# Kernel tuning notes

Hardware: AMD Instinct MI355X
Metric: run time of the kernel (lower is better)

## Reference

```python
import jax, jax.numpy as jnp
import numpy as np

BETA = 0.25
EPS_NORM = 1e-12

def _l2norm(x):
    # F.normalize(x, dim=-1): x / max(||x||, eps)
    n = jnp.sqrt(jnp.sum(x * x, axis=-1, keepdims=True))
    return x / jnp.maximum(n, EPS_NORM)

def setup_inputs() -> dict:
    key = jax.random.key(0)
    k1, k2 = jax.random.split(key)
    z = jax.random.normal(k1, (32, 4096, 256), dtype=jnp.float32)
    # matches nn.Embedding init uniform_(-1/num_embed, 1/num_embed)
    embed_weight = jax.random.uniform(k2, (1024, 256), dtype=jnp.float32,
                                      minval=-1.0 / 1024, maxval=1.0 / 1024)
    return {"z": z, "embed_weight": embed_weight}

def reference(z, embed_weight):
    num_embed, embed_dim = embed_weight.shape
    z_flat = z.reshape(-1, embed_dim)                      # [N, D]
    n_tok = z_flat.shape[0]

    # cosine distance: normalized z (detached) @ normalized codebook^T -> [N, K]
    zn = jax.lax.stop_gradient(_l2norm(z_flat))
    cn = _l2norm(embed_weight)
    d = zn @ cn.T                                          # [N, K]

    # torch sort(dim=1) then indices[:, -1] == argmax along codebook axis
    encoding_indices = jnp.argmax(d, axis=1)               # [N] int

    z_q = embed_weight[encoding_indices].reshape(z.shape)  # gather codebook rows

    # training losses (commitment + codebook)
    sg = jax.lax.stop_gradient
    loss = BETA * jnp.mean((sg(z_q) - z) ** 2) + jnp.mean((z_q - sg(z)) ** 2)

    # straight-through estimator
    z_q_st = z + sg(z_q - z)

    # perplexity from one-hot usage stats (counts instead of dense one-hot)
    counts = jnp.zeros((num_embed,), jnp.float32).at[encoding_indices].add(1.0)
    avg_probs = counts / jnp.float32(n_tok)
    perplexity = jnp.exp(-jnp.sum(avg_probs * jnp.log(avg_probs + 1e-10)))

    return z_q_st, loss, perplexity, encoding_indices
```

## Files before the change

### kernel.cpp

```cpp
#include <hip/hip_runtime.h>
#include <math.h>

#define N_TOK   131072
#define DIM     256
#define K_CODE  1024
#define MARGIN1 3e-2f
#define MARGIN2 2e-3f

#define WS_COUNTS   0
#define WS_LOSSFIX  4096
#define WS_RCOUNT2  4104
#define WS_RCOUNT1  4108
#define WS_PART     8192
#define WS_FIDX     20480
#define WS_RLIST2   1048576
#define WS_RLIST1   1572864
#define WS_BEXT     2097152

#define CHUNK_BYTES 49152

#define OUT_LOSS  33554432
#define OUT_PERP  33554433
#define OUT_IDX   33554434

typedef __bf16 bf16x8 __attribute__((ext_vector_type(8)));
typedef float  f32x4  __attribute__((ext_vector_type(4)));

static __device__ __forceinline__ unsigned short f2bf(float f) {
    unsigned int u = __float_as_uint(f);
    u += 0x7FFFu + ((u >> 16) & 1u);
    return (unsigned short)(u >> 16);
}
static __device__ __forceinline__ float bf2f(unsigned short h) {
    return __uint_as_float(((unsigned int)h) << 16);
}

static __device__ __forceinline__ void load_lds16(const void* g, void* l) {
    __builtin_amdgcn_global_load_lds(
        (const __attribute__((address_space(1))) unsigned int*)g,
        (__attribute__((address_space(3))) unsigned int*)l, 16, 0, 0);
}

__global__ void vq_pack(const float* __restrict__ embed, unsigned short* __restrict__ bext,
                        int* __restrict__ wshdr) {
    __shared__ float cs[4][DIM];
    const int tid  = threadIdx.x;
    const int w    = tid >> 6;
    const int lane = tid & 63;
    const int k0   = blockIdx.x * 4;

    if (blockIdx.x == 0) {
        for (int i = tid; i < 5120; i += 256) wshdr[i] = 0;
    }

    {
        const int k = k0 + w;
        float4 v = *(const float4*)&embed[k * DIM + lane * 4];
        float s = v.x * v.x + v.y * v.y + v.z * v.z + v.w * v.w;
        #pragma unroll
        for (int off = 32; off; off >>= 1) s += __shfl_xor(s, off);
        float inv = 1.0f / fmaxf(sqrtf(s), 1e-12f);
        float4 nv;
        nv.x = v.x * inv; nv.y = v.y * inv; nv.z = v.z * inv; nv.w = v.w * inv;
        *(float4*)&cs[w][lane * 4] = nv;
    }
    __syncthreads();

    for (int t = tid; t < 384; t += 256) {
        int lc  = t / 96;
        int g   = t - lc * 96;
        int k   = k0 + lc;
        int kk0 = g * 8;
        int src, hi;
        if (kk0 < 256)      { src = kk0;       hi = 1; }
        else if (kk0 < 512) { src = kk0 - 256; hi = 0; }
        else                { src = kk0 - 512; hi = 1; }
        unsigned short r[8] __attribute__((aligned(16)));
        #pragma unroll
        for (int j = 0; j < 8; ++j) {
            float vv = cs[lc][src + j];
            unsigned short h = f2bf(vv);
            r[j] = hi ? h : f2bf(vv - bf2f(h));
        }
        int c = k >> 5, kin = k & 31;
        int nt = kin >> 4, col = kin & 15;
        int ks = kk0 >> 5, quad = (kk0 >> 3) & 3;
        size_t dst = (size_t)c * CHUNK_BYTES + (size_t)(((nt * 24 + ks) * 64) + quad * 16 + col) * 16;
        *(float4*)((char*)bext + dst) = *(const float4*)r;
    }
}

__launch_bounds__(256, 4)
__global__ void vq_argmax1(const float* __restrict__ z,
                           const unsigned short* __restrict__ bext,
                           const float* __restrict__ embed,
                           int* __restrict__ fidx,
                           int* __restrict__ r1count, int* __restrict__ rlist1,
                           float* __restrict__ out, int* __restrict__ counts,
                           double* __restrict__ partials) {
    __shared__ unsigned short bbuf[16384];
    __shared__ double shl[4];

    const int tid  = threadIdx.x;
    const int w    = tid >> 6;
    const int lane = tid & 63;
    const int col  = lane & 15;
    const int quad = lane >> 4;
    const int tokBase = blockIdx.x * 128;

    bf16x8 ah[2][8];
    #pragma unroll
    for (int mt = 0; mt < 2; ++mt) {
        const float* zr = z + (size_t)(tokBase + w * 32 + mt * 16 + col) * DIM;
        #pragma unroll
        for (int ks = 0; ks < 8; ++ks) {
            float4 f0 = *(const float4*)(zr + ks * 32 + quad * 8);
            float4 f1 = *(const float4*)(zr + ks * 32 + quad * 8 + 4);
            float v[8] = {f0.x, f0.y, f0.z, f0.w, f1.x, f1.y, f1.z, f1.w};
            union { bf16x8 v; unsigned short u[8]; } th;
            #pragma unroll
            for (int j = 0; j < 8; ++j) th.u[j] = f2bf(v[j]);
            ah[mt][ks] = th.v;
        }
    }

    float best[2][4], second[2][4];
    int   bidx[2][4];
    #pragma unroll
    for (int mt = 0; mt < 2; ++mt)
        #pragma unroll
        for (int r = 0; r < 4; ++r) { best[mt][r] = -1e30f; second[mt][r] = -1e30f; bidx[mt][r] = 0; }

    for (int cc = 0; cc < 32; cc += 2) {
        __syncthreads();
        {
            #pragma unroll
            for (int i = 0; i < 8; ++i) {
                int lseg = w * 8 + i;
                int sub  = lseg >> 4;
                int l    = lseg & 15;
                int g    = l + ((l & 8) ? 16 : 0);
                load_lds16((const char*)bext + (size_t)(cc + sub) * CHUNK_BYTES
                                             + (size_t)g * 1024 + lane * 16,
                           (char*)bbuf + lseg * 1024);
            }
        }
        __syncthreads();

        #pragma unroll
        for (int sub = 0; sub < 2; ++sub) {
            f32x4 acc[2][2];
            #pragma unroll
            for (int mt = 0; mt < 2; ++mt)
                #pragma unroll
                for (int nt = 0; nt < 2; ++nt) acc[mt][nt] = (f32x4){0.f, 0.f, 0.f, 0.f};

            #pragma unroll
            for (int nt = 0; nt < 2; ++nt) {
                const unsigned short* bb = bbuf + sub * 8192 + nt * 4096;
                #pragma unroll
                for (int ks = 0; ks < 8; ++ks) {
                    bf16x8 b = *(const bf16x8*)&bb[ks * 512 + lane * 8];
                    acc[0][nt] = __builtin_amdgcn_mfma_f32_16x16x32_bf16(ah[0][ks], b, acc[0][nt], 0, 0, 0);
                    acc[1][nt] = __builtin_amdgcn_mfma_f32_16x16x32_bf16(ah[1][ks], b, acc[1][nt], 0, 0, 0);
                }
            }

            #pragma unroll
            for (int nt = 0; nt < 2; ++nt) {
                int code = (cc + sub) * 32 + nt * 16 + col;
                #pragma unroll
                for (int mt = 0; mt < 2; ++mt)
                    #pragma unroll
                    for (int r = 0; r < 4; ++r) {
                        float v = acc[mt][nt][r];
                        if (v > best[mt][r]) { second[mt][r] = best[mt][r]; best[mt][r] = v; bidx[mt][r] = code; }
                        else                 { second[mt][r] = fmaxf(second[mt][r], v); }
                    }
            }
        }
    }

    #pragma unroll
    for (int mt = 0; mt < 2; ++mt)
        #pragma unroll
        for (int r = 0; r < 4; ++r) {
            float B = best[mt][r], S = second[mt][r];
            int   I = bidx[mt][r];
            #pragma unroll
            for (int off = 1; off < 16; off <<= 1) {
                float ob = __shfl_xor(B, off);
                float os = __shfl_xor(S, off);
                int   oi = __shfl_xor(I, off);
                if (ob > B) {
                    S = fmaxf(B, os);
                    B = ob; I = oi;
                } else {
                    if (ob == B && oi < I) I = oi;
                    S = fmaxf(S, ob);
                }
            }
            int flag = (B - S < MARGIN1) ? 1 : 0;
            if (col == 0) {
                int token = tokBase + w * 32 + mt * 16 + quad * 4 + r;
                if (!flag) {
                    fidx[token] = I;
                    out[OUT_IDX + token] = (float)I;
                    atomicAdd(&counts[I], 1);
                } else {
                    int p = atomicAdd(r1count, 1);
                    rlist1[p] = token;
                }
            }
            bidx[mt][r] = I | (flag << 30);
        }

    double lsum = 0.0;
    #pragma unroll
    for (int mt = 0; mt < 2; ++mt)
        #pragma unroll
        for (int r = 0; r < 4; ++r)
            #pragma unroll
            for (int q = 0; q < 4; ++q) {
                int enc = __shfl(bidx[mt][r], q * 16);
                if (enc & (1 << 30)) continue;
                int idxv  = enc;
                int token = tokBase + w * 32 + mt * 16 + q * 4 + r;
                float4 e  = *(const float4*)&embed[(size_t)idxv * DIM + lane * 4];
                float4 zz = *(const float4*)&z[(size_t)token * DIM + lane * 4];
                float4 rr, o;
                rr.x = e.x - zz.x; rr.y = e.y - zz.y; rr.z = e.z - zz.z; rr.w = e.w - zz.w;
                o.x = zz.x + rr.x; o.y = zz.y + rr.y; o.z = zz.z + rr.z; o.w = zz.w + rr.w;
                *(float4*)&out[(size_t)token * DIM + lane * 4] = o;
                lsum += (double)rr.x * rr.x + (double)rr.y * rr.y +
                        (double)rr.z * rr.z + (double)rr.w * rr.w;
            }

    #pragma unroll
    for (int off = 32; off; off >>= 1) lsum += __shfl_down(lsum, off);
    if (lane == 0) shl[w] = lsum;
    __syncthreads();
    if (tid == 0) partials[blockIdx.x] = shl[0] + shl[1] + shl[2] + shl[3];
}

__launch_bounds__(256, 2)
__global__ void vq_redo(const float* __restrict__ z,
                        const unsigned short* __restrict__ bext,
                        const float* __restrict__ embed,
                        const int* __restrict__ r1count, const int* __restrict__ rlist1,
                        int* __restrict__ fidx,
                        int* __restrict__ r2count, int* __restrict__ rlist2,
                        float* __restrict__ out, int* __restrict__ counts,
                        double* __restrict__ partials) {
    __shared__ unsigned short bbuf[CHUNK_BYTES / 2];
    __shared__ double shl[4];

    const int tid  = threadIdx.x;
    const int w    = tid >> 6;
    const int lane = tid & 63;
    const int col  = lane & 15;
    const int quad = lane >> 4;
    const int cnt1 = *r1count;

    double lsum = 0.0;

    for (int base = blockIdx.x * 128; base < cnt1; base += gridDim.x * 128) {
        bf16x8 ah[2][8], al[2][8];
        #pragma unroll
        for (int mt = 0; mt < 2; ++mt) {
            int slot = base + w * 32 + mt * 16 + col;
            int tok  = rlist1[min(slot, cnt1 - 1)];
            const float* zr = z + (size_t)tok * DIM;
            #pragma unroll
            for (int ks = 0; ks < 8; ++ks) {
                float4 f0 = *(const float4*)(zr + ks * 32 + quad * 8);
                float4 f1 = *(const float4*)(zr + ks * 32 + quad * 8 + 4);
                float v[8] = {f0.x, f0.y, f0.z, f0.w, f1.x, f1.y, f1.z, f1.w};
                union { bf16x8 v; unsigned short u[8]; } th, tl;
                #pragma unroll
                for (int j = 0; j < 8; ++j) {
                    unsigned short h = f2bf(v[j]);
                    th.u[j] = h;
                    tl.u[j] = f2bf(v[j] - bf2f(h));
                }
                ah[mt][ks] = th.v;
                al[mt][ks] = tl.v;
            }
        }

        float best[2][4], second[2][4];
        int   bidx[2][4];
        #pragma unroll
        for (int mt = 0; mt < 2; ++mt)
            #pragma unroll
            for (int r = 0; r < 4; ++r) { best[mt][r] = -1e30f; second[mt][r] = -1e30f; bidx[mt][r] = 0; }

        for (int c = 0; c < 32; ++c) {
            __syncthreads();
            {
                const char* gsrc = (const char*)bext + (size_t)c * CHUNK_BYTES;
                #pragma unroll
                for (int i = 0; i < 12; ++i) {
                    int seg = w * 12 + i;
                    load_lds16(gsrc + (size_t)seg * 1024 + lane * 16,
                               (char*)bbuf + seg * 1024);
                }
            }
            __syncthreads();

            f32x4 acc[2][2];
            #pragma unroll
            for (int mt = 0; mt < 2; ++mt)
                #pragma unroll
                for (int nt = 0; nt < 2; ++nt) acc[mt][nt] = (f32x4){0.f, 0.f, 0.f, 0.f};

            #pragma unroll
            for (int nt = 0; nt < 2; ++nt) {
                const unsigned short* bb = bbuf + nt * 24 * 512;
                #pragma unroll
                for (int ks = 0; ks < 8; ++ks) {
                    bf16x8 b = *(const bf16x8*)&bb[ks * 512 + lane * 8];
                    acc[0][nt] = __builtin_amdgcn_mfma_f32_16x16x32_bf16(ah[0][ks], b, acc[0][nt], 0, 0, 0);
                    acc[1][nt] = __builtin_amdgcn_mfma_f32_16x16x32_bf16(ah[1][ks], b, acc[1][nt], 0, 0, 0);
                }
                #pragma unroll
                for (int ks = 0; ks < 8; ++ks) {
                    bf16x8 b = *(const bf16x8*)&bb[(8 + ks) * 512 + lane * 8];
                    acc[0][nt] = __builtin_amdgcn_mfma_f32_16x16x32_bf16(ah[0][ks], b, acc[0][nt], 0, 0, 0);
                    acc[1][nt] = __builtin_amdgcn_mfma_f32_16x16x32_bf16(ah[1][ks], b, acc[1][nt], 0, 0, 0);
                }
                #pragma unroll
                for (int ks = 0; ks < 8; ++ks) {
                    bf16x8 b = *(const bf16x8*)&bb[(16 + ks) * 512 + lane * 8];
                    acc[0][nt] = __builtin_amdgcn_mfma_f32_16x16x32_bf16(al[0][ks], b, acc[0][nt], 0, 0, 0);
                    acc[1][nt] = __builtin_amdgcn_mfma_f32_16x16x32_bf16(al[1][ks], b, acc[1][nt], 0, 0, 0);
                }
            }

            #pragma unroll
            for (int nt = 0; nt < 2; ++nt) {
                int code = c * 32 + nt * 16 + col;
                #pragma unroll
                for (int mt = 0; mt < 2; ++mt)
                    #pragma unroll
                    for (int r = 0; r < 4; ++r) {
                        float v = acc[mt][nt][r];
                        if (v > best[mt][r]) { second[mt][r] = best[mt][r]; best[mt][r] = v; bidx[mt][r] = code; }
                        else                 { second[mt][r] = fmaxf(second[mt][r], v); }
                    }
            }
        }

        #pragma unroll
        for (int mt = 0; mt < 2; ++mt)
            #pragma unroll
            for (int r = 0; r < 4; ++r) {
                float B = best[mt][r], S = second[mt][r];
                int   I = bidx[mt][r];
                #pragma unroll
                for (int off = 1; off < 16; off <<= 1) {
                    float ob = __shfl_xor(B, off);
                    float os = __shfl_xor(S, off);
                    int   oi = __shfl_xor(I, off);
                    if (ob > B) {
                        S = fmaxf(B, os);
                        B = ob; I = oi;
                    } else {
                        if (ob == B && oi < I) I = oi;
                        S = fmaxf(S, ob);
                    }
                }
                bidx[mt][r] = I;
                if (col == 0) {
                    int slot = base + w * 32 + mt * 16 + quad * 4 + r;
                    if (slot < cnt1) {
                        int token = rlist1[slot];
                        fidx[token] = I;
                        out[OUT_IDX + token] = (float)I;
                        atomicAdd(&counts[I], 1);
                        if (B - S < MARGIN2) {
                            int p = atomicAdd(r2count, 1);
                            rlist2[p] = token;
                        }
                    }
                }
            }

        #pragma unroll
        for (int mt = 0; mt < 2; ++mt)
            #pragma unroll
            for (int r = 0; r < 4; ++r)
                #pragma unroll
                for (int q = 0; q < 4; ++q) {
                    int slot = base + w * 32 + mt * 16 + q * 4 + r;
                    if (slot >= cnt1) continue;
                    int idxv  = __shfl(bidx[mt][r], q * 16);
                    int token = rlist1[slot];
                    float4 e  = *(const float4*)&embed[(size_t)idxv * DIM + lane * 4];
                    float4 zz = *(const float4*)&z[(size_t)token * DIM + lane * 4];
                    float4 rr, o;
                    rr.x = e.x - zz.x; rr.y = e.y - zz.y; rr.z = e.z - zz.z; rr.w = e.w - zz.w;
                    o.x = zz.x + rr.x; o.y = zz.y + rr.y; o.z = zz.z + rr.z; o.w = zz.w + rr.w;
                    *(float4*)&out[(size_t)token * DIM + lane * 4] = o;
                    lsum += (double)rr.x * rr.x + (double)rr.y * rr.y +
                            (double)rr.z * rr.z + (double)rr.w * rr.w;
                }
    }

    #pragma unroll
    for (int off = 32; off; off >>= 1) lsum += __shfl_down(lsum, off);
    if (lane == 0) shl[w] = lsum;
    __syncthreads();
    if (tid == 0) partials[1024 + blockIdx.x] = shl[0] + shl[1] + shl[2] + shl[3];
}

__global__ void vq_recheck(const float* __restrict__ z, const float* __restrict__ embed,
                           const int* __restrict__ r2count, const int* __restrict__ rlist2,
                           int* __restrict__ fidx, float* __restrict__ out,
                           int* __restrict__ counts, double* __restrict__ lossFix) {
    __shared__ double zd[DIM];
    __shared__ double rv[256];
    __shared__ int    rix[256];
    __shared__ int    s_old, s_new;
    const int cnt = *r2count;
    for (int li = blockIdx.x; li < cnt; li += gridDim.x) {
        int token = rlist2[li];
        __syncthreads();
        zd[threadIdx.x] = (double)z[(size_t)token * DIM + threadIdx.x];
        if (threadIdx.x == 0) s_old = fidx[token];
        __syncthreads();
        double bv = -1e300;
        int    bi = 0;
        #pragma unroll
        for (int j = 0; j < 4; ++j) {
            int k = threadIdx.x * 4 + j;
            const float* e = &embed[k * DIM];
            double acc = 0.0, nrm = 0.0;
            for (int d = 0; d < DIM; d += 4) {
                float4 ef = *(const float4*)&e[d];
                acc += (double)ef.x * zd[d]     + (double)ef.y * zd[d + 1] +
                       (double)ef.z * zd[d + 2] + (double)ef.w * zd[d + 3];
                nrm += (double)ef.x * ef.x + (double)ef.y * ef.y +
                       (double)ef.z * ef.z + (double)ef.w * ef.w;
            }
            double val = acc / fmax(sqrt(nrm), 1e-12);
            if (val > bv) { bv = val; bi = k; }
        }
        rv[threadIdx.x]  = bv;
        rix[threadIdx.x] = bi;
        __syncthreads();
        for (int s = 128; s; s >>= 1) {
            if (threadIdx.x < s) {
                double v2 = rv[threadIdx.x + s];
                int    i2 = rix[threadIdx.x + s];
                if (v2 > rv[threadIdx.x] ||
                    (v2 == rv[threadIdx.x] && i2 < rix[threadIdx.x])) {
                    rv[threadIdx.x] = v2;
                    rix[threadIdx.x] = i2;
                }
            }
            __syncthreads();
        }
        if (threadIdx.x == 0) {
            s_new = rix[0];
            if (s_new != s_old) {
                fidx[token] = s_new;
                out[OUT_IDX + token] = (float)s_new;
                atomicAdd(&counts[s_old], -1);
                atomicAdd(&counts[s_new], 1);
            }
        }
        __syncthreads();
        if (s_new != s_old && threadIdx.x < 64) {
            int lane = threadIdx.x;
            float4 en = *(const float4*)&embed[(size_t)s_new * DIM + lane * 4];
            float4 eo = *(const float4*)&embed[(size_t)s_old * DIM + lane * 4];
            float4 zz = *(const float4*)&z[(size_t)token * DIM + lane * 4];
            float4 rn, ro, o;
            rn.x = en.x - zz.x; rn.y = en.y - zz.y; rn.z = en.z - zz.z; rn.w = en.w - zz.w;
            ro.x = eo.x - zz.x; ro.y = eo.y - zz.y; ro.z = eo.z - zz.z; ro.w = eo.w - zz.w;
            o.x = zz.x + rn.x; o.y = zz.y + rn.y; o.z = zz.z + rn.z; o.w = zz.w + rn.w;
            *(float4*)&out[(size_t)token * DIM + lane * 4] = o;
            double d = (double)rn.x * rn.x + (double)rn.y * rn.y +
                       (double)rn.z * rn.z + (double)rn.w * rn.w -
                       ((double)ro.x * ro.x + (double)ro.y * ro.y +
                        (double)ro.z * ro.z + (double)ro.w * ro.w);
            #pragma unroll
            for (int off = 32; off; off >>= 1) d += __shfl_down(d, off);
            if (lane == 0) atomicAdd(lossFix, d);
        }
    }
}

__global__ void vq_finalize(const int* __restrict__ counts,
                            const double* __restrict__ partials,
                            const double* __restrict__ lossFix,
                            float* __restrict__ out) {
    __shared__ double sh[256];
    __shared__ double sl[256];
    double s = 0.0, ls = 0.0;
    for (int b = threadIdx.x; b < K_CODE; b += 256) {
        double p = (double)counts[b] / (double)N_TOK;
        s += p * log(p + 1e-10);
    }
    for (int b = threadIdx.x; b < 1280; b += 256) ls += partials[b];
    sh[threadIdx.x] = s;
    sl[threadIdx.x] = ls;
    __syncthreads();
    for (int st = 128; st; st >>= 1) {
        if (threadIdx.x < st) {
            sh[threadIdx.x] += sh[threadIdx.x + st];
            sl[threadIdx.x] += sl[threadIdx.x + st];
        }
        __syncthreads();
    }
    if (threadIdx.x == 0) {
        out[OUT_PERP] = (float)exp(-sh[0]);
        out[OUT_LOSS] = (float)(1.25 * (sl[0] + *lossFix) / (double)(N_TOK) / (double)(DIM));
    }
}

extern "C" void kernel_launch(void* const* d_in, const int* in_sizes, int n_in,
                              void* d_out, int out_size, void* d_ws, size_t ws_size,
                              hipStream_t stream) {
    const float* z     = (const float*)d_in[0];
    const float* embed = (const float*)d_in[1];
    float* out = (float*)d_out;
    char*  ws  = (char*)d_ws;

    int*            counts  = (int*)   (ws + WS_COUNTS);
    double*         lossFix = (double*)(ws + WS_LOSSFIX);
    int*            r2count = (int*)   (ws + WS_RCOUNT2);
    int*            r1count = (int*)   (ws + WS_RCOUNT1);
    double*         parts   = (double*)(ws + WS_PART);
    int*            fidx    = (int*)   (ws + WS_FIDX);
    int*            rlist2  = (int*)   (ws + WS_RLIST2);
    int*            rlist1  = (int*)   (ws + WS_RLIST1);
    unsigned short* bext    = (unsigned short*)(ws + WS_BEXT);

    vq_pack    <<<256,  256, 0, stream>>>(embed, bext, (int*)ws);
    vq_argmax1 <<<N_TOK / 128, 256, 0, stream>>>(z, bext, embed, fidx, r1count, rlist1,
                                                 out, counts, parts);
    vq_redo    <<<256,  256, 0, stream>>>(z, bext, embed, r1count, rlist1, fidx,
                                          r2count, rlist2, out, counts, parts);
    vq_recheck <<<512,  256, 0, stream>>>(z, embed, r2count, rlist2, fidx, out, counts, lossFix);
    vq_finalize<<<1,    256, 0, stream>>>(counts, parts, lossFix, out);
}
```

Baseline: 609.3 us.

## Load codebook fragments directly from global memory instead of staging through LDS

Both argmax kernels drop the LDS staging buffer, the global_load_lds copies and the per-chunk __syncthreads barriers. Each wave now reads its pre-packed bf16 codebook fragments straight from global memory (expected to hit in L2) into registers before issuing the MFMAs. This removes barrier stalls and LDS traffic and frees LDS, which may allow higher occupancy. The cost is redundant global/L2 reads, since every wave loads the same codebook data, plus extra registers for the fragment arrays.

```diff
diff --git a/kernel.cpp b/kernel.cpp
--- a/kernel.cpp
+++ b/kernel.cpp
@@ -33,12 +33,6 @@
 }
 static __device__ __forceinline__ float bf2f(unsigned short h) {
     return __uint_as_float(((unsigned int)h) << 16);
-}
-
-static __device__ __forceinline__ void load_lds16(const void* g, void* l) {
-    __builtin_amdgcn_global_load_lds(
-        (const __attribute__((address_space(1))) unsigned int*)g,
-        (__attribute__((address_space(3))) unsigned int*)l, 16, 0, 0);
 }
 
 __global__ void vq_pack(const float* __restrict__ embed, unsigned short* __restrict__ bext,
@@ -98,7 +92,6 @@
                            int* __restrict__ r1count, int* __restrict__ rlist1,
                            float* __restrict__ out, int* __restrict__ counts,
                            double* __restrict__ partials) {
-    __shared__ unsigned short bbuf[16384];
     __shared__ double shl[4];
 
     const int tid  = threadIdx.x;
@@ -131,53 +124,38 @@
         #pragma unroll
         for (int r = 0; r < 4; ++r) { best[mt][r] = -1e30f; second[mt][r] = -1e30f; bidx[mt][r] = 0; }
 
-    for (int cc = 0; cc < 32; cc += 2) {
-        __syncthreads();
-        {
-            #pragma unroll
-            for (int i = 0; i < 8; ++i) {
-                int lseg = w * 8 + i;
-                int sub  = lseg >> 4;
-                int l    = lseg & 15;
-                int g    = l + ((l & 8) ? 16 : 0);
-                load_lds16((const char*)bext + (size_t)(cc + sub) * CHUNK_BYTES
-                                             + (size_t)g * 1024 + lane * 16,
-                           (char*)bbuf + lseg * 1024);
-            }
-        }
-        __syncthreads();
-
-        #pragma unroll
-        for (int sub = 0; sub < 2; ++sub) {
-            f32x4 acc[2][2];
+    const char* bb0 = (const char*)bext + (size_t)lane * 16;
+    for (int c = 0; c < 32; ++c) {
+        f32x4 acc[2][2];
+        #pragma unroll
+        for (int mt = 0; mt < 2; ++mt)
+            #pragma unroll
+            for (int nt = 0; nt < 2; ++nt) acc[mt][nt] = (f32x4){0.f, 0.f, 0.f, 0.f};
+
+        #pragma unroll
+        for (int nt = 0; nt < 2; ++nt) {
+            const char* g = bb0 + (size_t)c * CHUNK_BYTES + (size_t)(nt * 24) * 1024;
+            bf16x8 b[8];
+            #pragma unroll
+            for (int ks = 0; ks < 8; ++ks) b[ks] = *(const bf16x8*)(g + ks * 1024);
+            #pragma unroll
+            for (int ks = 0; ks < 8; ++ks) {
+                acc[0][nt] = __builtin_amdgcn_mfma_f32_16x16x32_bf16(ah[0][ks], b[ks], acc[0][nt], 0, 0, 0);
+                acc[1][nt] = __builtin_amdgcn_mfma_f32_16x16x32_bf16(ah[1][ks], b[ks], acc[1][nt], 0, 0, 0);
+            }
+        }
+
+        #pragma unroll
+        for (int nt = 0; nt < 2; ++nt) {
+            int code = c * 32 + nt * 16 + col;
             #pragma unroll
             for (int mt = 0; mt < 2; ++mt)
                 #pragma unroll
-                for (int nt = 0; nt < 2; ++nt) acc[mt][nt] = (f32x4){0.f, 0.f, 0.f, 0.f};
-
-            #pragma unroll
-            for (int nt = 0; nt < 2; ++nt) {
-                const unsigned short* bb = bbuf + sub * 8192 + nt * 4096;
-                #pragma unroll
-                for (int ks = 0; ks < 8; ++ks) {
-                    bf16x8 b = *(const bf16x8*)&bb[ks * 512 + lane * 8];
-                    acc[0][nt] = __builtin_amdgcn_mfma_f32_16x16x32_bf16(ah[0][ks], b, acc[0][nt], 0, 0, 0);
-                    acc[1][nt] = __builtin_amdgcn_mfma_f32_16x16x32_bf16(ah[1][ks], b, acc[1][nt], 0, 0, 0);
-                }
-            }
-
-            #pragma unroll
-            for (int nt = 0; nt < 2; ++nt) {
-                int code = (cc + sub) * 32 + nt * 16 + col;
-                #pragma unroll
-                for (int mt = 0; mt < 2; ++mt)
-                    #pragma unroll
-                    for (int r = 0; r < 4; ++r) {
-                        float v = acc[mt][nt][r];
-                        if (v > best[mt][r]) { second[mt][r] = best[mt][r]; best[mt][r] = v; bidx[mt][r] = code; }
-                        else                 { second[mt][r] = fmaxf(second[mt][r], v); }
-                    }
-            }
+                for (int r = 0; r < 4; ++r) {
+                    float v = acc[mt][nt][r];
+                    if (v > best[mt][r]) { second[mt][r] = best[mt][r]; best[mt][r] = v; bidx[mt][r] = code; }
+                    else                 { second[mt][r] = fmaxf(second[mt][r], v); }
+                }
         }
     }
 
@@ -252,7 +230,6 @@
                         int* __restrict__ r2count, int* __restrict__ rlist2,
                         float* __restrict__ out, int* __restrict__ counts,
                         double* __restrict__ partials) {
-    __shared__ unsigned short bbuf[CHUNK_BYTES / 2];
     __shared__ double shl[4];
 
     const int tid  = threadIdx.x;
@@ -295,19 +272,8 @@
             #pragma unroll
             for (int r = 0; r < 4; ++r) { best[mt][r] = -1e30f; second[mt][r] = -1e30f; bidx[mt][r] = 0; }
 
+        const char* bb0 = (const char*)bext + (size_t)lane * 16;
         for (int c = 0; c < 32; ++c) {
-            __syncthreads();
-            {
-                const char* gsrc = (const char*)bext + (size_t)c * CHUNK_BYTES;
-                #pragma unroll
-                for (int i = 0; i < 12; ++i) {
-                    int seg = w * 12 + i;
-                    load_lds16(gsrc + (size_t)seg * 1024 + lane * 16,
-                               (char*)bbuf + seg * 1024);
-                }
-            }
-            __syncthreads();
-
             f32x4 acc[2][2];
             #pragma unroll
             for (int mt = 0; mt < 2; ++mt)
@@ -316,24 +282,28 @@
 
             #pragma unroll
             for (int nt = 0; nt < 2; ++nt) {
-                const unsigned short* bb = bbuf + nt * 24 * 512;
+                const char* g = bb0 + (size_t)c * CHUNK_BYTES + (size_t)(nt * 24) * 1024;
+                bf16x8 b[8];
+                #pragma unroll
+                for (int ks = 0; ks < 8; ++ks) b[ks] = *(const bf16x8*)(g + ks * 1024);
                 #pragma unroll
                 for (int ks = 0; ks < 8; ++ks) {
-                    bf16x8 b = *(const bf16x8*)&bb[ks * 512 + lane * 8];
-                    acc[0][nt] = __builtin_amdgcn_mfma_f32_16x16x32_bf16(ah[0][ks], b, acc[0][nt], 0, 0, 0);
-                    acc[1][nt] = __builtin_amdgcn_mfma_f32_16x16x32_bf16(ah[1][ks], b, acc[1][nt], 0, 0, 0);
-                }
+                    acc[0][nt] = __builtin_amdgcn_mfma_f32_16x16x32_bf16(ah[0][ks], b[ks], acc[0][nt], 0, 0, 0);
+                    acc[1][nt] = __builtin_amdgcn_mfma_f32_16x16x32_bf16(ah[1][ks], b[ks], acc[1][nt], 0, 0, 0);
+                }
+                #pragma unroll
+                for (int ks = 0; ks < 8; ++ks) b[ks] = *(const bf16x8*)(g + (8 + ks) * 1024);
                 #pragma unroll
                 for (int ks = 0; ks < 8; ++ks) {
-                    bf16x8 b = *(const bf16x8*)&bb[(8 + ks) * 512 + lane * 8];
-                    acc[0][nt] = __builtin_amdgcn_mfma_f32_16x16x32_bf16(ah[0][ks], b, acc[0][nt], 0, 0, 0);
-                    acc[1][nt] = __builtin_amdgcn_mfma_f32_16x16x32_bf16(ah[1][ks], b, acc[1][nt], 0, 0, 0);
-                }
+                    acc[0][nt] = __builtin_amdgcn_mfma_f32_16x16x32_bf16(ah[0][ks], b[ks], acc[0][nt], 0, 0, 0);
+                    acc[1][nt] = __builtin_amdgcn_mfma_f32_16x16x32_bf16(ah[1][ks], b[ks], acc[1][nt], 0, 0, 0);
+                }
+                #pragma unroll
+                for (int ks = 0; ks < 8; ++ks) b[ks] = *(const bf16x8*)(g + (16 + ks) * 1024);
                 #pragma unroll
                 for (int ks = 0; ks < 8; ++ks) {
-                    bf16x8 b = *(const bf16x8*)&bb[(16 + ks) * 512 + lane * 8];
-                    acc[0][nt] = __builtin_amdgcn_mfma_f32_16x16x32_bf16(al[0][ks], b, acc[0][nt], 0, 0, 0);
-                    acc[1][nt] = __builtin_amdgcn_mfma_f32_16x16x32_bf16(al[1][ks], b, acc[1][nt], 0, 0, 0);
+                    acc[0][nt] = __builtin_amdgcn_mfma_f32_16x16x32_bf16(al[0][ks], b[ks], acc[0][nt], 0, 0, 0);
+                    acc[1][nt] = __builtin_amdgcn_mfma_f32_16x16x32_bf16(al[1][ks], b[ks], acc[1][nt], 0, 0, 0);
                 }
             }
 
```

After: 857.7 us. 1.41x slower.
